# Optimization experiments

Hardware: AMD Instinct MI355X
Metric: run time of the kernel (lower is better)

## Reference

```python
import jax, jax.numpy as jnp
import numpy as np

BATCH, LENGTH, HIDDEN, SSM = 32, 2048, 128, 256


def setup_inputs() -> dict:
    key = jax.random.key(0)
    ks = jax.random.split(key, 7)
    b_std = 1.0 / np.sqrt(HIDDEN)
    c_std = 1.0 / np.sqrt(SSM)
    return {
        "inputs": jax.random.normal(ks[0], (BATCH, LENGTH, HIDDEN), jnp.float32),
        "A_diag": jax.random.normal(ks[1], (SSM,), jnp.float32),
        "G_diag": jax.random.uniform(ks[2], (SSM,), jnp.float32),
        "steps": jax.random.normal(ks[3], (SSM,), jnp.float32) * 0.5,
        "B": jax.random.uniform(ks[4], (SSM, HIDDEN, 2), jnp.float32, -b_std, b_std),
        "C": jax.random.uniform(ks[5], (HIDDEN, SSM, 2), jnp.float32, -c_std, c_std),
        "D": jax.random.normal(ks[6], (HIDDEN,), jnp.float32),
    }


def _project_parameters(A_diag, G_diag, steps):
    # Mirrors DampedLinOSSLayer._project_parameters: sigmoid step, relu damping,
    # and clamp A into the band where the 2x2 IMEX1 transition has complex eigenvalues.
    step = jax.nn.sigmoid(steps)
    g = jax.nn.relu(G_diag)
    denom = jnp.maximum(step * step, 1e-6)
    s = step * g
    base = jnp.sqrt(jnp.maximum(1.0 + s, 1e-6))
    a_low = (2.0 + s - 2.0 * base) / denom
    a_high = (2.0 + s + 2.0 * base) / denom
    a = a_low + jax.nn.relu(A_diag - a_low) - jax.nn.relu(A_diag - a_high)
    return a, g, step


def _eigenvalue(a, g, step):
    # IMEX1 transition M = [[S, -S*dt*A], [dt*S, 1 - dt^2*S*A]] with S = 1/(1+dt*G).
    # det(M) = S, trace(M) = S + 1 - dt^2*S*A; projection guarantees trace^2 < 4*det,
    # so eigenvalues form a conjugate pair lam = T/2 + i*sqrt(S - T^2/4).
    S = 1.0 / (1.0 + step * g)
    T = S + 1.0 - step * step * S * a
    imag = jnp.sqrt(jnp.maximum(S - 0.25 * T * T, 0.0))
    return jax.lax.complex(0.5 * T, imag)  # [P] complex64


def reference(inputs, A_diag, G_diag, steps, B, C, D):
    a, g, step = _project_parameters(A_diag, G_diag, steps)
    lam = _eigenvalue(a, g, step)  # [P]

    # Complex input projection: bu = (B_re + i*B_im) @ u, shape [batch, L, P]
    bu = jax.lax.complex(
        jnp.einsum("blh,ph->blp", inputs, B[..., 0]),
        jnp.einsum("blh,ph->blp", inputs, B[..., 1]),
    )

    # Diagonal complex linear recurrence x_k = lam * x_{k-1} + bu_k via associative scan.
    def combine(e1, e2):
        a1, b1 = e1
        a2, b2 = e2
        return a1 * a2, a2 * b1 + b2

    lam_b = jnp.broadcast_to(lam[None, None, :], bu.shape)
    _, states = jax.lax.associative_scan(combine, (lam_b, bu), axis=1)

    # Output: Re(C @ x) + D * u
    projected = (
        jnp.einsum("blp,hp->blh", states.real, C[..., 0])
        - jnp.einsum("blp,hp->blh", states.imag, C[..., 1])
    )
    return projected + inputs * D
```

## Files before the change

### kernel.cpp

```cpp
#include <hip/hip_runtime.h>
#include <hip/hip_bf16.h>
#include <math.h>

#define BATCH 32
#define LEN   2048
#define HID   128
#define SSM   256

#define BPL 32768

typedef __attribute__((ext_vector_type(4))) float f32x4;
typedef __attribute__((ext_vector_type(8))) short bf16x8;
typedef __attribute__((ext_vector_type(4))) int   i32x4;

static __device__ __forceinline__ unsigned short f2bf(float x) {
    union { float f; unsigned u; } v; v.f = x;
    unsigned r = (v.u + 0x7FFFu + ((v.u >> 16) & 1u)) >> 16;
    return (unsigned short)r;
}
static __device__ __forceinline__ unsigned short f2bf_hi(float x) {
    union { float f; unsigned u; } v; v.f = x;
    return (unsigned short)(v.u >> 16);
}
static __device__ __forceinline__ float bf2f(unsigned short b) {
    union { unsigned u; float f; } v; v.u = ((unsigned)b) << 16;
    return v.f;
}
static __device__ __forceinline__ unsigned int cvtpk(float a, float b) {
    __hip_bfloat162 h = __float22bfloat162_rn(float2{a, b});
    union { __hip_bfloat162 h2; unsigned int u; } c; c.h2 = h;
    return c.u;
}
static __device__ __forceinline__ void cmul(float& rr, float& ri,
                                            float ar, float ai, float br, float bi) {
    rr = ar * br - ai * bi;
    ri = ar * bi + ai * br;
}
static __device__ __forceinline__ void gload16(const void* g, void* l) {
    __builtin_amdgcn_global_load_lds(
        (const __attribute__((address_space(1))) unsigned int*)g,
        (__attribute__((address_space(3))) unsigned int*)l,
        16, 0, 0);
}

__global__ __launch_bounds__(256) void kprep(const float* __restrict__ u,
                                             const float* __restrict__ Bm,
                                             const float* __restrict__ Cm,
                                             const float* __restrict__ A,
                                             const float* __restrict__ G,
                                             const float* __restrict__ steps,
                                             unsigned short* __restrict__ ubf,
                                             unsigned short* __restrict__ Bsp,
                                             unsigned short* __restrict__ C2,
                                             float* __restrict__ lam) {
    if (blockIdx.x < 2048) {
        const int total = BATCH * LEN * HID;
        const int stride = 2048 * 256 * 8;
        for (int i = (blockIdx.x * 256 + threadIdx.x) * 8; i < total; i += stride) {
            f32x4 a = *(const f32x4*)&u[i];
            f32x4 c = *(const f32x4*)&u[i + 4];
            i32x4 o;
            o[0] = (int)cvtpk(a[0], a[1]);
            o[1] = (int)cvtpk(a[2], a[3]);
            o[2] = (int)cvtpk(c[0], c[1]);
            o[3] = (int)cvtpk(c[2], c[3]);
            *(i32x4*)&ubf[i] = o;
        }
        return;
    }
    if (blockIdx.x == 2304) {
        int p = threadIdx.x;
        if (p < SSM) {
            float stp   = 1.f / (1.f + expf(-steps[p]));
            float g     = fmaxf(G[p], 0.f);
            float denom = fmaxf(stp * stp, 1e-6f);
            float s     = stp * g;
            float base  = sqrtf(fmaxf(1.f + s, 1e-6f));
            float alow  = (2.f + s - 2.f * base) / denom;
            float ahigh = (2.f + s + 2.f * base) / denom;
            float a     = alow + fmaxf(A[p] - alow, 0.f) - fmaxf(A[p] - ahigh, 0.f);
            float S     = 1.f / (1.f + stp * g);
            float T     = S + 1.f - stp * stp * S * a;
            lam[p]       = 0.5f * T;
            lam[SSM + p] = sqrtf(fmaxf(S - 0.25f * T * T, 0.f));
        }
        return;
    }
    int gidx = (blockIdx.x - 2048) * 256 + threadIdx.x;
    if (gidx < 32768) {
        int p = gidx >> 7, h = gidx & 127;
        float vr = Bm[(size_t)(p * HID + h) * 2];
        float vi = Bm[(size_t)(p * HID + h) * 2 + 1];
        unsigned short hh = f2bf_hi(vr);
        Bsp[0 * BPL + p * HID + h] = hh;
        Bsp[1 * BPL + p * HID + h] = f2bf(vr - bf2f(hh));
        hh = f2bf_hi(vi);
        Bsp[2 * BPL + p * HID + h] = hh;
        Bsp[3 * BPL + p * HID + h] = f2bf(vi - bf2f(hh));
    } else {
        int g2 = gidx - 32768;
        int h = g2 >> 8, p = g2 & 255;
        float vr = Cm[(size_t)(h * SSM + p) * 2];
        float vi = -Cm[(size_t)(h * SSM + p) * 2 + 1];
        unsigned short rh = f2bf_hi(vr);
        unsigned short ih = f2bf_hi(vi);
        size_t rowh = (size_t)h * 512;
        C2[rowh + 2 * p]               = rh;
        C2[rowh + 2 * p + 1]           = ih;
        C2[65536 + rowh + 2 * p]       = f2bf(vr - bf2f(rh));
        C2[65536 + rowh + 2 * p + 1]   = f2bf(vi - bf2f(ih));
    }
}

__global__ __launch_bounds__(512, 4) void k12_fused(const unsigned short* __restrict__ ubf,
                                                    const unsigned short* __restrict__ Bsp,
                                                    const float* __restrict__ lam,
                                                    unsigned short* __restrict__ TP) {
    __shared__ __align__(16) char sU[2][32768];
    __shared__ __align__(16) char sT2[10240];
    __shared__ float Rld[4][2][8][2];

    int d    = blockIdx.x;
    int xcd  = d & 7;
    int idx  = d >> 3;
    int pt   = idx & 15;
    int bhi  = idx >> 4;
    int b    = bhi * 8 + xcd;
    int p0   = pt * 16;

    int tid  = threadIdx.x;
    int lane = tid & 63, w = tid >> 6;
    int wl   = w >> 1, wp = w & 1;
    int fr   = lane & 15, g = lane >> 4;
    int frp  = fr & 7;
    int comp = fr >> 3;
    int pcol = p0 + wp * 8 + frp;

    const unsigned short* Bh  = Bsp + (size_t)(comp * 2) * BPL + (size_t)pcol * HID;
    const unsigned short* Blo = Bsp + (size_t)(comp * 2 + 1) * BPL + (size_t)pcol * HID;
    bf16x8 Bfh[4], Bfl[4];
#pragma unroll
    for (int kc = 0; kc < 4; ++kc) {
        Bfh[kc] = *(const bf16x8*)&Bh[kc * 32 + g * 8];
        Bfl[kc] = *(const bf16x8*)&Blo[kc * 32 + g * 8];
    }

    float pw_r[4], pw_i[4];
    float lg_r, lg_i;
    float l4r, l4i, l8r, l8i, l16r, l16i, l32r, l32i;
    {
        float ar = lam[pcol], ai = lam[SSM + pcol];
        pw_r[0] = ar; pw_i[0] = ai;
        cmul(pw_r[1], pw_i[1], ar, ai, ar, ai);
        cmul(pw_r[2], pw_i[2], pw_r[1], pw_i[1], ar, ai);
        cmul(pw_r[3], pw_i[3], pw_r[1], pw_i[1], pw_r[1], pw_i[1]);
        l4r = pw_r[3]; l4i = pw_i[3];
        cmul(l8r, l8i, l4r, l4i, l4r, l4i);
        cmul(l16r, l16i, l8r, l8i, l8r, l8i);
        cmul(l32r, l32i, l16r, l16i, l16r, l16i);
        if (g == 0)      { lg_r = 1.f; lg_i = 0.f; }
        else if (g == 1) { lg_r = l4r; lg_i = l4i; }
        else if (g == 2) { lg_r = l8r; lg_i = l8i; }
        else             { cmul(lg_r, lg_i, l8r, l8i, l4r, l4i); }
    }

    float TCr = 0.f, TCi = 0.f;

    const unsigned short* ub = ubf + (size_t)b * (LEN * HID);
    int srow32  = tid >> 4;
    int stg_src = srow32 * HID + ((((tid & 15) * 16) ^ ((srow32 & 7) << 4)) >> 1);

#define STAGE(buf, tt)                                                        \
    {                                                                         \
        const unsigned short* gs = ub + (size_t)(tt) * 16384 + stg_src;       \
        char* ls = &sU[buf][tid * 16];                                        \
        _Pragma("unroll")                                                     \
        for (int q = 0; q < 4; ++q)                                           \
            gload16(gs + q * 4096, ls + q * 8192);                            \
    }

    STAGE(0, 0)
    __syncthreads();
    int cur = 0;

    for (int t = 0; t < 16; ++t) {
        int l0t = t * 128;

        if (t < 15) STAGE(cur ^ 1, t + 1)

        const char* su = &sU[cur][0];
        f32x4 acc[2];
        acc[0] = (f32x4)(0.f); acc[1] = (f32x4)(0.f);
#pragma unroll
        for (int kc = 0; kc < 4; ++kc) {
#pragma unroll
            for (int mi = 0; mi < 2; ++mi) {
                int off = (wl * 32 + mi * 16 + fr) * 256 + ((kc * 64 + g * 16) ^ ((fr & 7) << 4));
                bf16x8 ah = *(const bf16x8*)(su + off);
                acc[mi] = __builtin_amdgcn_mfma_f32_16x16x32_bf16(ah, Bfh[kc], acc[mi], 0, 0, 0);
                acc[mi] = __builtin_amdgcn_mfma_f32_16x16x32_bf16(ah, Bfl[kc], acc[mi], 0, 0, 0);
            }
        }

        float xr[4], xi[4];
#pragma unroll
        for (int e = 0; e < 4; ++e) {
            float send = (comp == 0) ? acc[1][e] : acc[0][e];
            float oth  = __shfl_xor(send, 8, 64);
            xr[e] = (comp == 0) ? acc[0][e] : oth;
            xi[e] = (comp == 0) ? oth       : acc[1][e];
        }

        float Er, Ei, Fr, Fi, For, Foi;
        {
            float lr = pw_r[0], li = pw_i[0];
            float cr = 0.f, ci = 0.f;
#pragma unroll
            for (int r = 0; r < 4; ++r) {
                float nr = fmaf(lr, cr, fmaf(-li, ci, xr[r]));
                float ni = fmaf(lr, ci, fmaf(li, cr, xi[r]));
                cr = nr; ci = ni;
                xr[r] = cr; xi[r] = ci;
            }
            float Qr = cr, Qi = ci;
            float ur = __shfl_up(Qr, 16u, 64);
            float ui = __shfl_up(Qi, 16u, 64);
            if (g >= 1) {
                Qr = fmaf(l4r, ur, fmaf(-l4i, ui, Qr));
                Qi = fmaf(l4r, ui, fmaf(l4i, ur, Qi));
            }
            ur = __shfl_up(Qr, 32u, 64);
            ui = __shfl_up(Qi, 32u, 64);
            if (g >= 2) {
                Qr = fmaf(l8r, ur, fmaf(-l8i, ui, Qr));
                Qi = fmaf(l8r, ui, fmaf(l8i, ur, Qi));
            }
            Er = __shfl_up(Qr, 16u, 64);
            Ei = __shfl_up(Qi, 16u, 64);
            if (g == 0) { Er = 0.f; Ei = 0.f; }
            Fr = __shfl(Qr, fr + 48, 64);
            Fi = __shfl(Qi, fr + 48, 64);
            For = __shfl_xor(Fr, 8, 64);
            Foi = __shfl_xor(Fi, 8, 64);
            float Rr = fmaf(l16r, For, fmaf(-l16i, Foi, Fr));
            float Ri = fmaf(l16r, Foi, fmaf(l16i, For, Fi));
            if (g == 0 && fr >= 8) { Rld[wl][wp][frp][0] = Rr; Rld[wl][wp][frp][1] = Ri; }
        }
        asm volatile("s_waitcnt lgkmcnt(0)" ::: "memory");
        __builtin_amdgcn_s_barrier();
        __builtin_amdgcn_sched_barrier(0);

        {
            float Wr = TCr, Wi = TCi;
            float Tr = TCr, Ti = TCi;
#pragma unroll
            for (int w2 = 0; w2 < 4; ++w2) {
                float rr = Rld[w2][wp][frp][0], ri = Rld[w2][wp][frp][1];
                float nTr = fmaf(l32r, Tr, fmaf(-l32i, Ti, rr));
                float nTi = fmaf(l32r, Ti, fmaf(l32i, Tr, ri));
                Tr = nTr; Ti = nTi;
                if (w2 < wl) {
                    float nWr = fmaf(l32r, Wr, fmaf(-l32i, Wi, rr));
                    float nWi = fmaf(l32r, Wi, fmaf(l32i, Wr, ri));
                    Wr = nWr; Wi = nWi;
                }
            }
            TCr = Tr; TCi = Ti;
            float prr, pri;
            if (comp == 0) { prr = Wr; pri = Wi; }
            else {
                prr = fmaf(l16r, Wr, fmaf(-l16i, Wi, For));
                pri = fmaf(l16r, Wi, fmaf(l16i, Wr, Foi));
            }
            float Mr = fmaf(lg_r, prr, fmaf(-lg_i, pri, Er));
            float Mi = fmaf(lg_r, pri, fmaf(lg_i, prr, Ei));
#pragma unroll
            for (int r = 0; r < 4; ++r) {
                xr[r] = fmaf(pw_r[r], Mr, fmaf(-pw_i[r], Mi, xr[r]));
                xi[r] = fmaf(pw_r[r], Mi, fmaf(pw_i[r], Mr, xi[r]));
            }
        }

        {
            int colb  = wl * 32 + comp * 16 + g * 4;
            int idxu  = wp * 8 + frp;
            int piece = idxu >> 2, sub = idxu & 3;
            int pw    = piece ^ g;
#pragma unroll
            for (int r = 0; r < 4; ++r) {
                unsigned int pk = cvtpk(xr[r], xi[r]);
                *(unsigned int*)(sT2 + (colb + r) * 80 + pw * 16 + sub * 4) = pk;
            }
        }
        __syncthreads();

        {
            int row = tid >> 2, q = tid & 3;
            int x2  = (row >> 2) & 3;
            bf16x8 v = *(const bf16x8*)(sT2 + row * 80 + ((q ^ x2) * 16));
            *(bf16x8*)&TP[((size_t)(b * LEN) + l0t + row) * 512 + p0 * 2 + q * 8] = v;
        }
        cur ^= 1;
    }
#undef STAGE
}

__global__ __launch_bounds__(512, 4) void k3_out(const unsigned short* __restrict__ TP,
                                                 const unsigned short* __restrict__ C2,
                                                 const unsigned short* __restrict__ ubf,
                                                 const float* __restrict__ D,
                                                 float* __restrict__ out) {
    __shared__ __align__(16) char sAB[3][24576];

    int d    = blockIdx.x;
    int xcd  = d & 7;
    int rest = d >> 3;
    int lt   = rest & 15;
    int bhi  = rest >> 4;
    int b    = bhi * 8 + xcd;
    int l0   = lt * 128;

    int tid = threadIdx.x;
    int lane = tid & 63, w = tid >> 6;
    int wl = w >> 1, wh = w & 1;
    int fr = lane & 15, g = lane >> 4;

    f32x4 acc[2][4];
#pragma unroll
    for (int mi = 0; mi < 2; ++mi)
#pragma unroll
        for (int ni = 0; ni < 4; ++ni) acc[mi][ni] = (f32x4)(0.f);

    float dv[4];
#pragma unroll
    for (int ni = 0; ni < 4; ++ni) dv[ni] = D[wh * 64 + ni * 16 + fr];

#define STAGE3(buf, cc)                                                       \
    {                                                                         \
        {                                                                     \
            int rw = tid >> 2, sl = tid & 3;                                  \
            gload16(TP + ((size_t)(b * LEN) + l0 + rw) * 512 + (cc) * 32 +    \
                        ((sl ^ (rw & 3)) * 8),                                \
                    &sAB[buf][tid * 16]);                                     \
        }                                                                     \
        _Pragma("unroll")                                                     \
        for (int q = 0; q < 2; ++q) {                                         \
            int dg = tid + q * 512;                                           \
            int hl = dg >> 9, hr = (dg >> 2) & 127, sl = dg & 3;              \
            gload16(C2 + ((size_t)(hl * 128 + hr)) * 512 + (cc) * 32 +        \
                        ((sl ^ (hr & 3)) * 8),                                \
                    &sAB[buf][8192 + dg * 16]);                               \
        }                                                                     \
    }

    STAGE3(0, 0)
    __syncthreads();
    STAGE3(1, 1)

    int cur = 0;
    for (int c = 0; c < 16; ++c) {
        if (c < 14) STAGE3((cur + 2) % 3, c + 2)

        const char* sb = &sAB[cur][0];
        int swz = (g ^ (fr & 3)) * 16;
        bf16x8 af[2];
#pragma unroll
        for (int mi = 0; mi < 2; ++mi) {
            int arow = wl * 32 + mi * 16 + fr;
            af[mi] = *(const bf16x8*)(sb + arow * 64 + swz);
        }
#pragma unroll
        for (int ni = 0; ni < 4; ++ni) {
            int hrow = wh * 64 + ni * 16 + fr;
            bf16x8 ch = *(const bf16x8*)(sb + 8192 + hrow * 64 + swz);
            bf16x8 cl = *(const bf16x8*)(sb + 8192 + 8192 + hrow * 64 + swz);
#pragma unroll
            for (int mi = 0; mi < 2; ++mi) {
                acc[mi][ni] = __builtin_amdgcn_mfma_f32_16x16x32_bf16(af[mi], ch, acc[mi][ni], 0, 0, 0);
                acc[mi][ni] = __builtin_amdgcn_mfma_f32_16x16x32_bf16(af[mi], cl, acc[mi][ni], 0, 0, 0);
            }
        }
        if (c < 14) {
            asm volatile("s_waitcnt vmcnt(3) lgkmcnt(0)" ::: "memory");
        } else {
            asm volatile("s_waitcnt vmcnt(0) lgkmcnt(0)" ::: "memory");
        }
        __builtin_amdgcn_s_barrier();
        __builtin_amdgcn_sched_barrier(0);
        cur = (cur + 1) % 3;
    }
#undef STAGE3

#pragma unroll
    for (int mi = 0; mi < 2; ++mi)
#pragma unroll
        for (int ni = 0; ni < 4; ++ni) {
            int lb = l0 + wl * 32 + mi * 16 + g * 4;
            int h  = wh * 64 + ni * 16 + fr;
#pragma unroll
            for (int r = 0; r < 4; ++r) {
                size_t idx = ((size_t)b * LEN + lb + r) * HID + h;
                out[idx] = acc[mi][ni][r] + bf2f(ubf[idx]) * dv[ni];
            }
        }
}

extern "C" void kernel_launch(void* const* d_in, const int* in_sizes, int n_in,
                              void* d_out, int out_size, void* d_ws, size_t ws_size,
                              hipStream_t stream) {
    const float* u  = (const float*)d_in[0];
    const float* A  = (const float*)d_in[1];
    const float* G  = (const float*)d_in[2];
    const float* st = (const float*)d_in[3];
    const float* B  = (const float*)d_in[4];
    const float* C  = (const float*)d_in[5];
    const float* D  = (const float*)d_in[6];
    float* out = (float*)d_out;

    char* WS = (char*)d_ws;
    unsigned short* TP  = (unsigned short*)WS;
    float* lam          = (float*)(WS + 67108864);
    unsigned short* Bsp = (unsigned short*)(WS + 67110912);
    unsigned short* C2  = (unsigned short*)(WS + 67373056);
    unsigned short* ubf = (unsigned short*)(WS + 67635200);

    kprep<<<2305, 256, 0, stream>>>(u, B, C, A, G, st, ubf, Bsp, C2, lam);
    k12_fused<<<512, 512, 0, stream>>>(ubf, Bsp, lam, TP);
    k3_out<<<512, 512, 0, stream>>>(TP, C2, ubf, D, out);
}
```

Measured before the change: 81.71 us.

## Drop LDS transpose staging, double-buffer scan carries, split MFMA accumulators

```diff
diff --git a/kernel.cpp b/kernel.cpp
--- a/kernel.cpp
+++ b/kernel.cpp
@@ -117,8 +117,7 @@
                                                     const float* __restrict__ lam,
                                                     unsigned short* __restrict__ TP) {
     __shared__ __align__(16) char sU[2][32768];
-    __shared__ __align__(16) char sT2[10240];
-    __shared__ float Rld[4][2][8][2];
+    __shared__ float Rld[2][4][2][8][2];
 
     int d    = blockIdx.x;
     int xcd  = d & 7;
@@ -183,24 +182,34 @@
     __syncthreads();
     int cur = 0;
 
+    int colb = wl * 32 + comp * 16 + g * 4;
+
     for (int t = 0; t < 16; ++t) {
         int l0t = t * 128;
 
         if (t < 15) STAGE(cur ^ 1, t + 1)
 
         const char* su = &sU[cur][0];
+        f32x4 accA[2], accB[2];
+        accA[0] = (f32x4)(0.f); accA[1] = (f32x4)(0.f);
+        accB[0] = (f32x4)(0.f); accB[1] = (f32x4)(0.f);
+#pragma unroll
+        for (int kc = 0; kc < 2; ++kc) {
+#pragma unroll
+            for (int mi = 0; mi < 2; ++mi) {
+                int off0 = (wl * 32 + mi * 16 + fr) * 256 + ((kc * 64 + g * 16) ^ ((fr & 7) << 4));
+                int off1 = (wl * 32 + mi * 16 + fr) * 256 + (((kc + 2) * 64 + g * 16) ^ ((fr & 7) << 4));
+                bf16x8 ah0 = *(const bf16x8*)(su + off0);
+                bf16x8 ah1 = *(const bf16x8*)(su + off1);
+                accA[mi] = __builtin_amdgcn_mfma_f32_16x16x32_bf16(ah0, Bfh[kc], accA[mi], 0, 0, 0);
+                accA[mi] = __builtin_amdgcn_mfma_f32_16x16x32_bf16(ah0, Bfl[kc], accA[mi], 0, 0, 0);
+                accB[mi] = __builtin_amdgcn_mfma_f32_16x16x32_bf16(ah1, Bfh[kc + 2], accB[mi], 0, 0, 0);
+                accB[mi] = __builtin_amdgcn_mfma_f32_16x16x32_bf16(ah1, Bfl[kc + 2], accB[mi], 0, 0, 0);
+            }
+        }
         f32x4 acc[2];
-        acc[0] = (f32x4)(0.f); acc[1] = (f32x4)(0.f);
-#pragma unroll
-        for (int kc = 0; kc < 4; ++kc) {
-#pragma unroll
-            for (int mi = 0; mi < 2; ++mi) {
-                int off = (wl * 32 + mi * 16 + fr) * 256 + ((kc * 64 + g * 16) ^ ((fr & 7) << 4));
-                bf16x8 ah = *(const bf16x8*)(su + off);
-                acc[mi] = __builtin_amdgcn_mfma_f32_16x16x32_bf16(ah, Bfh[kc], acc[mi], 0, 0, 0);
-                acc[mi] = __builtin_amdgcn_mfma_f32_16x16x32_bf16(ah, Bfl[kc], acc[mi], 0, 0, 0);
-            }
-        }
+        acc[0] = accA[0] + accB[0];
+        acc[1] = accA[1] + accB[1];
 
         float xr[4], xi[4];
 #pragma unroll
@@ -244,18 +253,16 @@
             Foi = __shfl_xor(Fi, 8, 64);
             float Rr = fmaf(l16r, For, fmaf(-l16i, Foi, Fr));
             float Ri = fmaf(l16r, Foi, fmaf(l16i, For, Fi));
-            if (g == 0 && fr >= 8) { Rld[wl][wp][frp][0] = Rr; Rld[wl][wp][frp][1] = Ri; }
-        }
-        asm volatile("s_waitcnt lgkmcnt(0)" ::: "memory");
-        __builtin_amdgcn_s_barrier();
-        __builtin_amdgcn_sched_barrier(0);
+            if (g == 0 && fr >= 8) { Rld[t & 1][wl][wp][frp][0] = Rr; Rld[t & 1][wl][wp][frp][1] = Ri; }
+        }
+        __syncthreads();
 
         {
             float Wr = TCr, Wi = TCi;
             float Tr = TCr, Ti = TCi;
 #pragma unroll
             for (int w2 = 0; w2 < 4; ++w2) {
-                float rr = Rld[w2][wp][frp][0], ri = Rld[w2][wp][frp][1];
+                float rr = Rld[t & 1][w2][wp][frp][0], ri = Rld[t & 1][w2][wp][frp][1];
                 float nTr = fmaf(l32r, Tr, fmaf(-l32i, Ti, rr));
                 float nTi = fmaf(l32r, Ti, fmaf(l32i, Tr, ri));
                 Tr = nTr; Ti = nTi;
@@ -282,23 +289,10 @@
         }
 
         {
-            int colb  = wl * 32 + comp * 16 + g * 4;
-            int idxu  = wp * 8 + frp;
-            int piece = idxu >> 2, sub = idxu & 3;
-            int pw    = piece ^ g;
-#pragma unroll
-            for (int r = 0; r < 4; ++r) {
-                unsigned int pk = cvtpk(xr[r], xi[r]);
-                *(unsigned int*)(sT2 + (colb + r) * 80 + pw * 16 + sub * 4) = pk;
-            }
-        }
-        __syncthreads();
-
-        {
-            int row = tid >> 2, q = tid & 3;
-            int x2  = (row >> 2) & 3;
-            bf16x8 v = *(const bf16x8*)(sT2 + row * 80 + ((q ^ x2) * 16));
-            *(bf16x8*)&TP[((size_t)(b * LEN) + l0t + row) * 512 + p0 * 2 + q * 8] = v;
+            size_t rowbase = ((size_t)(b * LEN) + l0t + colb) * 512 + pcol * 2;
+#pragma unroll
+            for (int r = 0; r < 4; ++r)
+                *(unsigned int*)&TP[rowbase + (size_t)r * 512] = cvtpk(xr[r], xi[r]);
         }
         cur ^= 1;
     }
```

After: 79.31 us. -2.9%, faster.
